# Kernel optimization log

Hardware: AMD Instinct MI355X
Metric: run time of the kernel (lower is better)

## Reference

```python
import jax, jax.numpy as jnp
import numpy as np

NUM_EXPERTS = 8
HIDDEN = 1024
INTER = 2816
T = 16          # tokens
TOP_K = 2       # active experts per token
INIT_STD = 0.02


def setup_inputs() -> dict:
    key = jax.random.key(0)
    k_x, k_idx, k_g, k_u, k_d = jax.random.split(key, 5)
    x = jax.random.normal(k_x, (T, HIDDEN), dtype=jnp.float32)
    expert_indices = jax.random.randint(k_idx, (T, TOP_K), 0, NUM_EXPERTS)
    gate_proj = INIT_STD * jax.random.normal(k_g, (NUM_EXPERTS, INTER, HIDDEN), dtype=jnp.float32)
    up_proj = INIT_STD * jax.random.normal(k_u, (NUM_EXPERTS, HIDDEN, INTER), dtype=jnp.float32)
    down_proj = INIT_STD * jax.random.normal(k_d, (NUM_EXPERTS, INTER, HIDDEN), dtype=jnp.float32)
    return {"x": x, "expert_indices": expert_indices,
            "gate_proj": gate_proj, "up_proj": up_proj, "down_proj": down_proj}


def reference(x, expert_indices, gate_proj, up_proj, down_proj):
    # Faithful to the torch module, including its swapped proj naming:
    #   gate branch: gate_proj[idx] : [t, a, I, H]
    #   'down' branch (acts as up): down_proj[idx] : [t, a, I, H]
    #   final contraction: up_proj[idx] : [t, a, H, I]
    gw = gate_proj[expert_indices]          # [t, a, I, H]
    dw = down_proj[expert_indices]          # [t, a, I, H]
    uw = up_proj[expert_indices]            # [t, a, H, I]
    x1 = jax.nn.silu(jnp.einsum('ti,taoi->tao', x, gw))  # [t, a, I]
    x3 = jnp.einsum('ti,taoi->tao', x, dw)               # [t, a, I]
    expert_outs = jnp.einsum('tao,taio->tai', x1 * x3, uw)  # [t, a, H]
    return expert_outs
```

## Files before the change

### kernel.cpp

```cpp
#include <hip/hip_runtime.h>

#define NE 8
#define HD 1024
#define IW 2816
#define NT 16
#define TK 2
#define NP (NT*TK)
#define NPC1 8
#define ROWS1 8
#define NPC2 4
#define ROWS2 2

#define LOADW(G, D, r) { _Pragma("unroll") \
    for (int c = 0; c < 4; ++c) { \
        float4 gv = *(const float4*)(gp + (size_t)(r) * HD + c * 256); \
        float4 dv = *(const float4*)(dp + (size_t)(r) * HD + c * 256); \
        G[4*c+0]=gv.x; G[4*c+1]=gv.y; G[4*c+2]=gv.z; G[4*c+3]=gv.w; \
        D[4*c+0]=dv.x; D[4*c+1]=dv.y; D[4*c+2]=dv.z; D[4*c+3]=dv.w; } }

#define COMPROW(G, D, r) { \
    float ag[NPC1], ad[NPC1]; \
    _Pragma("unroll") for (int j = 0; j < NPC1; ++j) { ag[j]=0.f; ad[j]=0.f; } \
    _Pragma("unroll") for (int j = 0; j < NPC1; ++j) if (j < nc) { \
        _Pragma("unroll") for (int c = 0; c < 4; ++c) { \
            float4 xv = *(const float4*)&s_x[j][c*256 + lane*4]; \
            ag[j] += xv.x*G[4*c+0] + xv.y*G[4*c+1] + xv.z*G[4*c+2] + xv.w*G[4*c+3]; \
            ad[j] += xv.x*D[4*c+0] + xv.y*D[4*c+1] + xv.z*D[4*c+2] + xv.w*D[4*c+3]; } } \
    _Pragma("unroll") for (int off = 32; off > 0; off >>= 1) { \
        _Pragma("unroll") for (int j = 0; j < NPC1; ++j) if (j < nc) { \
            ag[j] += __shfl_xor(ag[j], off, 64); \
            ad[j] += __shfl_xor(ad[j], off, 64); } } \
    if (lane == 0) { _Pragma("unroll") for (int j = 0; j < NPC1; ++j) if (j < nc) { \
        const float g = ag[j]; \
        const float s = g / (1.f + __expf(-g)); \
        hbuf[(size_t)s_list[g0 + j] * IW + (o0 + (r))] = s * ad[j]; } } }

__global__ __launch_bounds__(256) void moe_phase1(
    const float* __restrict__ x,
    const int*   __restrict__ idx,
    const float* __restrict__ gate,
    const float* __restrict__ down,
    float*       __restrict__ hbuf)
{
    __shared__ float s_x[NPC1][HD];
    __shared__ int s_list[NP];
    __shared__ int s_n;
    const int e = blockIdx.y;
    {
        const int t = threadIdx.x;
        const bool mine = (t < NP) && (idx[t] == e);
        const unsigned long long m = __ballot(mine);
        if (mine) s_list[__popcll(m & ((1ull << t) - 1ull))] = t;
        if (t == 0) s_n = (int)__popcll(m);
    }
    __syncthreads();
    const int npl = s_n;
    if (npl == 0) return;

    const int wave = threadIdx.x >> 6;
    const int lane = threadIdx.x & 63;
    const int o0 = (blockIdx.x * 4 + wave) * ROWS1;
    const float* gp = gate + ((size_t)e * IW + o0) * HD + lane * 4;
    const float* dp = down + ((size_t)e * IW + o0) * HD + lane * 4;

    for (int g0 = 0; g0 < npl; g0 += NPC1) {
        const int nc = (npl - g0 < NPC1) ? (npl - g0) : NPC1;
        __syncthreads();
        {
            const int t = threadIdx.x;
            for (int j = 0; j < nc; ++j) {
                const int tok = s_list[g0 + j] >> 1;
                *(float4*)&s_x[j][t * 4] = *(const float4*)(x + (size_t)tok * HD + t * 4);
            }
        }
        __syncthreads();

        float gA[16], dA[16], gB[16], dB[16];
        LOADW(gA, dA, 0);
        LOADW(gB, dB, 1);
        COMPROW(gA, dA, 0);
        LOADW(gA, dA, 2);
        COMPROW(gB, dB, 1);
        LOADW(gB, dB, 3);
        COMPROW(gA, dA, 2);
        LOADW(gA, dA, 4);
        COMPROW(gB, dB, 3);
        LOADW(gB, dB, 5);
        COMPROW(gA, dA, 4);
        LOADW(gA, dA, 6);
        COMPROW(gB, dB, 5);
        LOADW(gB, dB, 7);
        COMPROW(gA, dA, 6);
        COMPROW(gB, dB, 7);
    }
}

#define LOADU(W, r) { _Pragma("unroll") \
    for (int c = 0; c < 11; ++c) { \
        float4 uv = *(const float4*)(upp + (size_t)(r) * IW + c * 256); \
        W[4*c+0]=uv.x; W[4*c+1]=uv.y; W[4*c+2]=uv.z; W[4*c+3]=uv.w; } }

#define COMPH(W, r) { \
    float acc[NPC2]; \
    _Pragma("unroll") for (int j = 0; j < NPC2; ++j) acc[j] = 0.f; \
    _Pragma("unroll") for (int j = 0; j < NPC2; ++j) if (j < nc) { \
        _Pragma("unroll") for (int c = 0; c < 11; ++c) { \
            float4 hv = *(const float4*)&s_h[j][c*256 + lane*4]; \
            acc[j] += W[4*c+0]*hv.x + W[4*c+1]*hv.y + W[4*c+2]*hv.z + W[4*c+3]*hv.w; } } \
    _Pragma("unroll") for (int off = 32; off > 0; off >>= 1) { \
        _Pragma("unroll") for (int j = 0; j < NPC2; ++j) if (j < nc) \
            acc[j] += __shfl_xor(acc[j], off, 64); } \
    if (lane == 0) { _Pragma("unroll") for (int j = 0; j < NPC2; ++j) if (j < nc) \
        out[(size_t)s_list[g0 + j] * HD + (h0 + (r))] = acc[j]; } }

__global__ __launch_bounds__(256) void moe_phase2(
    const float* __restrict__ up,
    const int*   __restrict__ idx,
    const float* __restrict__ hbuf,
    float*       __restrict__ out)
{
    __shared__ float s_h[NPC2][IW];
    __shared__ int s_list[NP];
    __shared__ int s_n;
    const int e = blockIdx.y;
    {
        const int t = threadIdx.x;
        const bool mine = (t < NP) && (idx[t] == e);
        const unsigned long long m = __ballot(mine);
        if (mine) s_list[__popcll(m & ((1ull << t) - 1ull))] = t;
        if (t == 0) s_n = (int)__popcll(m);
    }
    __syncthreads();
    const int npl = s_n;
    if (npl == 0) return;

    const int wave = threadIdx.x >> 6;
    const int lane = threadIdx.x & 63;
    const int h0 = (blockIdx.x * 4 + wave) * ROWS2;
    const float* upp = up + ((size_t)e * HD + h0) * IW + lane * 4;

    for (int g0 = 0; g0 < npl; g0 += NPC2) {
        const int nc = (npl - g0 < NPC2) ? (npl - g0) : NPC2;
        __syncthreads();
        {
            const int t = threadIdx.x;
            for (int j = 0; j < nc; ++j) {
                const float* hr = hbuf + (size_t)s_list[g0 + j] * IW;
                for (int k = t; k < IW / 4; k += 256)
                    *(float4*)&s_h[j][k * 4] = *(const float4*)(hr + k * 4);
            }
        }
        __syncthreads();

        float wA[44], wB[44];
        LOADU(wA, 0);
        LOADU(wB, 1);
        COMPH(wA, 0);
        COMPH(wB, 1);
    }
}

extern "C" void kernel_launch(void* const* d_in, const int* in_sizes, int n_in,
                              void* d_out, int out_size, void* d_ws, size_t ws_size,
                              hipStream_t stream) {
    const float* x    = (const float*)d_in[0];
    const int*   idx  = (const int*)  d_in[1];
    const float* gate = (const float*)d_in[2];
    const float* up   = (const float*)d_in[3];
    const float* down = (const float*)d_in[4];
    float* hbuf = (float*)d_ws;
    float* out  = (float*)d_out;

    moe_phase1<<<dim3(IW / (4 * ROWS1), NE), dim3(256), 0, stream>>>(x, idx, gate, down, hbuf);
    moe_phase2<<<dim3(HD / (4 * ROWS2), NE), dim3(256), 0, stream>>>(up, idx, hbuf, out);
}
```

Before: 342.5 us.

## Restructure phase1 to keep weight rows in registers and read x directly

Phase 1 now gives each wave 2 rows instead of 8, so the grid has four times as many blocks. Each wave loads its gate and down weight rows into registers once, outside the token loop, instead of reloading them per token chunk. The shared-memory staging of x and its barriers are removed, and each wave reads token activations straight from global memory through the cache. This aims at more parallelism and fewer reloads of weights for experts with many tokens, at the cost of redundant x reads across waves and smaller token chunks (4 instead of 8).

```diff
diff --git a/kernel.cpp b/kernel.cpp
--- a/kernel.cpp
+++ b/kernel.cpp
@@ -6,34 +6,10 @@
 #define NT 16
 #define TK 2
 #define NP (NT*TK)
-#define NPC1 8
-#define ROWS1 8
+#define ROWS1 2
+#define NPC1 4
 #define NPC2 4
 #define ROWS2 2
-
-#define LOADW(G, D, r) { _Pragma("unroll") \
-    for (int c = 0; c < 4; ++c) { \
-        float4 gv = *(const float4*)(gp + (size_t)(r) * HD + c * 256); \
-        float4 dv = *(const float4*)(dp + (size_t)(r) * HD + c * 256); \
-        G[4*c+0]=gv.x; G[4*c+1]=gv.y; G[4*c+2]=gv.z; G[4*c+3]=gv.w; \
-        D[4*c+0]=dv.x; D[4*c+1]=dv.y; D[4*c+2]=dv.z; D[4*c+3]=dv.w; } }
-
-#define COMPROW(G, D, r) { \
-    float ag[NPC1], ad[NPC1]; \
-    _Pragma("unroll") for (int j = 0; j < NPC1; ++j) { ag[j]=0.f; ad[j]=0.f; } \
-    _Pragma("unroll") for (int j = 0; j < NPC1; ++j) if (j < nc) { \
-        _Pragma("unroll") for (int c = 0; c < 4; ++c) { \
-            float4 xv = *(const float4*)&s_x[j][c*256 + lane*4]; \
-            ag[j] += xv.x*G[4*c+0] + xv.y*G[4*c+1] + xv.z*G[4*c+2] + xv.w*G[4*c+3]; \
-            ad[j] += xv.x*D[4*c+0] + xv.y*D[4*c+1] + xv.z*D[4*c+2] + xv.w*D[4*c+3]; } } \
-    _Pragma("unroll") for (int off = 32; off > 0; off >>= 1) { \
-        _Pragma("unroll") for (int j = 0; j < NPC1; ++j) if (j < nc) { \
-            ag[j] += __shfl_xor(ag[j], off, 64); \
-            ad[j] += __shfl_xor(ad[j], off, 64); } } \
-    if (lane == 0) { _Pragma("unroll") for (int j = 0; j < NPC1; ++j) if (j < nc) { \
-        const float g = ag[j]; \
-        const float s = g / (1.f + __expf(-g)); \
-        hbuf[(size_t)s_list[g0 + j] * IW + (o0 + (r))] = s * ad[j]; } } }
 
 __global__ __launch_bounds__(256) void moe_phase1(
     const float* __restrict__ x,
@@ -42,7 +18,6 @@
     const float* __restrict__ down,
     float*       __restrict__ hbuf)
 {
-    __shared__ float s_x[NPC1][HD];
     __shared__ int s_list[NP];
     __shared__ int s_n;
     const int e = blockIdx.y;
@@ -60,38 +35,68 @@
     const int wave = threadIdx.x >> 6;
     const int lane = threadIdx.x & 63;
     const int o0 = (blockIdx.x * 4 + wave) * ROWS1;
+
     const float* gp = gate + ((size_t)e * IW + o0) * HD + lane * 4;
     const float* dp = down + ((size_t)e * IW + o0) * HD + lane * 4;
+    float gw[ROWS1][16], dw[ROWS1][16];
+    #pragma unroll
+    for (int r = 0; r < ROWS1; ++r) {
+        #pragma unroll
+        for (int c = 0; c < 4; ++c) {
+            float4 gv = *(const float4*)(gp + (size_t)r * HD + c * 256);
+            float4 dv = *(const float4*)(dp + (size_t)r * HD + c * 256);
+            gw[r][4*c+0]=gv.x; gw[r][4*c+1]=gv.y; gw[r][4*c+2]=gv.z; gw[r][4*c+3]=gv.w;
+            dw[r][4*c+0]=dv.x; dw[r][4*c+1]=dv.y; dw[r][4*c+2]=dv.z; dw[r][4*c+3]=dv.w;
+        }
+    }
 
-    for (int g0 = 0; g0 < npl; g0 += NPC1) {
-        const int nc = (npl - g0 < NPC1) ? (npl - g0) : NPC1;
-        __syncthreads();
-        {
-            const int t = threadIdx.x;
-            for (int j = 0; j < nc; ++j) {
-                const int tok = s_list[g0 + j] >> 1;
-                *(float4*)&s_x[j][t * 4] = *(const float4*)(x + (size_t)tok * HD + t * 4);
+    for (int n0 = 0; n0 < npl; n0 += NPC1) {
+        const int nc = (npl - n0 < NPC1) ? (npl - n0) : NPC1;
+        float ag[ROWS1][NPC1], ad[ROWS1][NPC1];
+        #pragma unroll
+        for (int r = 0; r < ROWS1; ++r)
+            #pragma unroll
+            for (int j = 0; j < NPC1; ++j) { ag[r][j] = 0.f; ad[r][j] = 0.f; }
+
+        #pragma unroll
+        for (int j = 0; j < NPC1; ++j) {
+            if (j < nc) {
+                const float* xrow = x + (size_t)(s_list[n0 + j] >> 1) * HD + lane * 4;
+                #pragma unroll
+                for (int c = 0; c < 4; ++c) {
+                    float4 xv = *(const float4*)(xrow + c * 256);
+                    #pragma unroll
+                    for (int r = 0; r < ROWS1; ++r) {
+                        ag[r][j] += xv.x*gw[r][4*c+0] + xv.y*gw[r][4*c+1]
+                                  + xv.z*gw[r][4*c+2] + xv.w*gw[r][4*c+3];
+                        ad[r][j] += xv.x*dw[r][4*c+0] + xv.y*dw[r][4*c+1]
+                                  + xv.z*dw[r][4*c+2] + xv.w*dw[r][4*c+3];
+                    }
+                }
             }
         }
-        __syncthreads();
-
-        float gA[16], dA[16], gB[16], dB[16];
-        LOADW(gA, dA, 0);
-        LOADW(gB, dB, 1);
-        COMPROW(gA, dA, 0);
-        LOADW(gA, dA, 2);
-        COMPROW(gB, dB, 1);
-        LOADW(gB, dB, 3);
-        COMPROW(gA, dA, 2);
-        LOADW(gA, dA, 4);
-        COMPROW(gB, dB, 3);
-        LOADW(gB, dB, 5);
-        COMPROW(gA, dA, 4);
-        LOADW(gA, dA, 6);
-        COMPROW(gB, dB, 5);
-        LOADW(gB, dB, 7);
-        COMPROW(gA, dA, 6);
-        COMPROW(gB, dB, 7);
+        #pragma unroll
+        for (int off = 32; off > 0; off >>= 1) {
+            #pragma unroll
+            for (int r = 0; r < ROWS1; ++r)
+                #pragma unroll
+                for (int j = 0; j < NPC1; ++j)
+                    if (j < nc) {
+                        ag[r][j] += __shfl_xor(ag[r][j], off, 64);
+                        ad[r][j] += __shfl_xor(ad[r][j], off, 64);
+                    }
+        }
+        if (lane == 0) {
+            #pragma unroll
+            for (int r = 0; r < ROWS1; ++r)
+                #pragma unroll
+                for (int j = 0; j < NPC1; ++j)
+                    if (j < nc) {
+                        const float g = ag[r][j];
+                        const float s = g / (1.f + __expf(-g));
+                        hbuf[(size_t)s_list[n0 + j] * IW + (o0 + r)] = s * ad[r][j];
+                    }
+        }
     }
 }
 
```

Result: faster. 286.1 us (-16.5%).
